# Performance work log

Measured on AMD Instinct MI355X. Metric: run time of the kernel, lower is better.

## Reference

```python
import jax, jax.numpy as jnp
import numpy as np

EPS = 1e-5
ALPHA = 0.7
N_HEADS = 20
N_KV_HEADS = 5
HEAD_DIM = 128


def bitlinear(x, w):
    # absmean ternary quantization per output row: w_t = sign(w)*(|w| > alpha*absmean)
    absw = jnp.abs(w)
    absmean = jnp.mean(absw, axis=1, keepdims=True)            # [out, 1]
    tern = jnp.sign(w) * (absw > ALPHA * absmean).astype(w.dtype)
    # (X @ pos^T - X @ neg^T) * scale == (X @ tern^T) * scale
    return jnp.einsum('...i,oi->...o', x, tern) * absmean[:, 0]


def rmsnorm(x, g):
    var = jnp.mean(jnp.square(x), axis=-1, keepdims=True)
    return x * jax.lax.rsqrt(var + EPS) * g


def rotate_half(x):
    x1, x2 = jnp.split(x, 2, axis=-1)
    return jnp.concatenate([-x2, x1], axis=-1)


def setup_inputs() -> dict:
    key = jax.random.key(0)
    ks = jax.random.split(key, 12)
    h, inter = 2560, 6912
    b, s = 1, 2048
    wscale = 1.0 / np.sqrt(h)
    return {
        'x': jax.random.normal(ks[0], (b, s, h), jnp.float32),
        'cos': jax.random.uniform(ks[1], (1, 1, s, HEAD_DIM), jnp.float32),
        'sin': jax.random.uniform(ks[2], (1, 1, s, HEAD_DIM), jnp.float32),
        'q_w': jax.random.normal(ks[3], (h, h), jnp.float32) * wscale,
        'k_w': jax.random.normal(ks[4], (N_KV_HEADS * HEAD_DIM, h), jnp.float32) * wscale,
        'v_w': jax.random.normal(ks[5], (N_KV_HEADS * HEAD_DIM, h), jnp.float32) * wscale,
        'o_w': jax.random.normal(ks[6], (h, h), jnp.float32) * wscale,
        'gate_w': jax.random.normal(ks[7], (inter, h), jnp.float32) * wscale,
        'up_w': jax.random.normal(ks[8], (inter, h), jnp.float32) * wscale,
        'down_w': jax.random.normal(ks[9], (h, inter), jnp.float32) / np.sqrt(inter),
        'ln1_w': jnp.ones((h,), jnp.float32),
        'ln2_w': jnp.ones((h,), jnp.float32),
    }


def reference(x, cos, sin, q_w, k_w, v_w, o_w, gate_w, up_w, down_w, ln1_w, ln2_w):
    b, s, hdim = x.shape
    residual = x
    h = rmsnorm(x, ln1_w)

    q = bitlinear(h, q_w).reshape(b, s, N_HEADS, HEAD_DIM).transpose(0, 2, 1, 3)
    k = bitlinear(h, k_w).reshape(b, s, N_KV_HEADS, HEAD_DIM).transpose(0, 2, 1, 3)
    v = bitlinear(h, v_w).reshape(b, s, N_KV_HEADS, HEAD_DIM).transpose(0, 2, 1, 3)

    # RoPE
    q = q * cos + rotate_half(q) * sin
    k = k * cos + rotate_half(k) * sin

    # GQA: repeat_interleave kv heads
    n_rep = N_HEADS // N_KV_HEADS
    k = jnp.repeat(k, n_rep, axis=1)
    v = jnp.repeat(v, n_rep, axis=1)

    scale = 1.0 / np.sqrt(HEAD_DIM)
    attn = jnp.einsum('bhqd,bhkd->bhqk', q, k) * scale
    attn = jax.nn.softmax(attn, axis=-1)
    o = jnp.einsum('bhqk,bhkd->bhqd', attn, v)
    o = o.transpose(0, 2, 1, 3).reshape(b, s, hdim)

    x = residual + bitlinear(o, o_w)

    residual = x
    h = rmsnorm(x, ln2_w)
    gate = jnp.square(jax.nn.relu(bitlinear(h, gate_w)))  # relu^2
    x = residual + bitlinear(gate * bitlinear(h, up_w), down_w)
    return x
```

## Files before the change

kernel.cpp:

```cpp
#include <hip/hip_runtime.h>
#include <hip/hip_bf16.h>

typedef unsigned short u16;
typedef short bf16x8 __attribute__((ext_vector_type(8)));
typedef float f32x4 __attribute__((ext_vector_type(4)));

__device__ __forceinline__ u16 f2b(float f) {
    union { __hip_bfloat16 h; u16 u; } cv;
    cv.h = __float2bfloat16(f);
    return cv.u;
}
__device__ __forceinline__ float b2f(u16 u) {
    union { u16 u; __hip_bfloat16 h; } cv;
    cv.u = u;
    return __bfloat162float(cv.h);
}

__device__ __forceinline__ void g2l16(const void* g, void* l) {
    __builtin_amdgcn_global_load_lds(
        (const __attribute__((address_space(1))) unsigned int*)g,
        (__attribute__((address_space(3))) unsigned int*)l, 16, 0, 0);
}

template <int EPT>
__global__ __launch_bounds__(256) void quant_kernel(const float* __restrict__ W,
                                                    u16* __restrict__ T,
                                                    float* __restrict__ scales, int K) {
    const int row = blockIdx.x, tid = threadIdx.x;
    const float* wr = W + (size_t)row * K;
    float v[EPT];
    float s = 0.f;
#pragma unroll
    for (int i = 0; i < EPT; ++i) { v[i] = wr[tid + i * 256]; s += fabsf(v[i]); }
#pragma unroll
    for (int d = 1; d < 64; d <<= 1) s += __shfl_xor(s, d);
    __shared__ float red[4];
    if ((tid & 63) == 0) red[tid >> 6] = s;
    __syncthreads();
    const float absmean = (red[0] + red[1] + red[2] + red[3]) / (float)K;
    const float thr = 0.7f * absmean;
    u16* tr = T + (size_t)row * K;
#pragma unroll
    for (int i = 0; i < EPT; ++i) {
        float w = v[i];
        float t = (fabsf(w) > thr) ? ((w > 0.f) ? 1.f : -1.f) : 0.f;
        tr[tid + i * 256] = f2b(t);
    }
    if (tid == 0) scales[row] = absmean;
}

__global__ __launch_bounds__(256) void rmsnorm_kernel(const float* __restrict__ x,
                                                      const float* __restrict__ g,
                                                      u16* __restrict__ o) {
    const int row = blockIdx.x, tid = threadIdx.x;
    const float* xr = x + (size_t)row * 2560;
    float v[10];
    float s = 0.f;
#pragma unroll
    for (int i = 0; i < 10; ++i) { v[i] = xr[tid + i * 256]; s += v[i] * v[i]; }
#pragma unroll
    for (int d = 1; d < 64; d <<= 1) s += __shfl_xor(s, d);
    __shared__ float red[4];
    if ((tid & 63) == 0) red[tid >> 6] = s;
    __syncthreads();
    const float total = red[0] + red[1] + red[2] + red[3];
    const float rs = rsqrtf(total * (1.f / 2560.f) + 1e-5f);
    u16* orow = o + (size_t)row * 2560;
#pragma unroll
    for (int i = 0; i < 10; ++i) orow[tid + i * 256] = f2b(v[i] * rs * g[tid + i * 256]);
}

template <int MODE>
__global__ __launch_bounds__(512, 4) void gemm_bt(const u16* __restrict__ A,
                                                  const u16* __restrict__ B,
                                                  const float* __restrict__ scale,
                                                  const float* __restrict__ res,
                                                  void* __restrict__ outp,
                                                  int M, int N, int K) {
    __shared__ __align__(16) u16 sA[128 * 64];
    __shared__ __align__(16) u16 sB[128 * 64];
    const int tid = threadIdx.x;
    const int wave = tid >> 6, lane = tid & 63;
    const int lane15 = lane & 15, quad = lane >> 4;
    const int m0 = blockIdx.x * 128, n0 = blockIdx.y * 128;
    const int wm = wave >> 2, wn = wave & 3;

    f32x4 acc[4][2] = {};

    const int r0 = wave * 8 + (lane >> 3);
    const int gcc = (lane & 7) ^ (lane >> 3);
    const size_t aoff = (size_t)(m0 + r0) * K + gcc * 8;
    const size_t boff = (size_t)(n0 + r0) * K + gcc * 8;
    char* ldsA = (char*)sA + wave * 1024;
    char* ldsB = (char*)sB + wave * 1024;
    const int sw = lane15 & 7;

    for (int kt = 0; kt < K; kt += 64) {
        g2l16(A + aoff + kt, ldsA);
        g2l16(A + aoff + (size_t)64 * K + kt, ldsA + 8192);
        g2l16(B + boff + kt, ldsB);
        g2l16(B + boff + (size_t)64 * K + kt, ldsB + 8192);
        __syncthreads();
#pragma unroll
        for (int kc = 0; kc < 2; ++kc) {
            const int pc = ((kc * 4 + quad) ^ sw) * 8;
            bf16x8 af[4], bfr[2];
#pragma unroll
            for (int f = 0; f < 4; ++f)
                af[f] = *(const bf16x8*)&sA[(wm * 64 + f * 16 + lane15) * 64 + pc];
#pragma unroll
            for (int f = 0; f < 2; ++f)
                bfr[f] = *(const bf16x8*)&sB[(wn * 32 + f * 16 + lane15) * 64 + pc];
#pragma unroll
            for (int i = 0; i < 4; ++i)
#pragma unroll
                for (int j = 0; j < 2; ++j)
                    acc[i][j] = __builtin_amdgcn_mfma_f32_16x16x32_bf16(af[i], bfr[j], acc[i][j], 0, 0, 0);
        }
        __syncthreads();
    }

#pragma unroll
    for (int j = 0; j < 2; ++j) {
        const int c = n0 + wn * 32 + j * 16 + lane15;
        const float sc = scale[c];
#pragma unroll
        for (int i = 0; i < 4; ++i) {
            const int rbase = m0 + wm * 64 + i * 16 + quad * 4;
#pragma unroll
            for (int r = 0; r < 4; ++r) {
                const float vv = acc[i][j][r] * sc;
                const size_t idx = (size_t)(rbase + r) * N + c;
                if (MODE == 0) ((u16*)outp)[idx] = f2b(vv);
                else           ((float*)outp)[idx] = res[idx] + vv;
            }
        }
    }
}

__global__ __launch_bounds__(256) void rope_kernel(u16* __restrict__ buf, int stride,
                                                   const float* __restrict__ cs,
                                                   const float* __restrict__ sn, int nh) {
    const int idx = blockIdx.x * 256 + threadIdx.x;
    const int d = idx & 63;
    const int h = (idx >> 6) % nh;
    const int s = idx / (64 * nh);
    const size_t base = (size_t)s * stride + h * 128;
    const float a = b2f(buf[base + d]), b = b2f(buf[base + d + 64]);
    const float c1 = cs[s * 128 + d], s1 = sn[s * 128 + d];
    const float c2 = cs[s * 128 + d + 64], s2 = sn[s * 128 + d + 64];
    buf[base + d] = f2b(a * c1 - b * s1);
    buf[base + d + 64] = f2b(b * c2 + a * s2);
}

__global__ __launch_bounds__(256) void transpose_v_kernel(const u16* __restrict__ V, int stride,
                                                          u16* __restrict__ VT) {
    __shared__ u16 t[128 * 66];
    const int tid = threadIdx.x;
    const int h = blockIdx.y, s0 = blockIdx.x * 64;
#pragma unroll
    for (int i = 0; i < 32; ++i) {
        const int idx = tid + i * 256;
        const int r = idx >> 7, c = idx & 127;
        t[c * 66 + r] = V[(size_t)(s0 + r) * stride + h * 128 + c];
    }
    __syncthreads();
#pragma unroll
    for (int i = 0; i < 32; ++i) {
        const int idx = tid + i * 256;
        const int d = idx >> 6, s = idx & 63;
        VT[((size_t)h * 128 + d) * 2048 + s0 + s] = t[d * 66 + s];
    }
}

__global__ __launch_bounds__(256, 3) void flash_kernel(const u16* __restrict__ Q, int qs,
                                                       const u16* __restrict__ Kb,
                                                       const u16* __restrict__ VT,
                                                       u16* __restrict__ O) {
    __shared__ __align__(16) u16 sQ[64 * 128];
    __shared__ __align__(16) u16 sK[2][32 * 128];
    __shared__ __align__(16) u16 sV[2][128 * 32];
    const int tid = threadIdx.x, wave = tid >> 6, lane = tid & 63;
    const int lane15 = lane & 15, quad = lane >> 4;
    const int head = blockIdx.y, q0 = blockIdx.x * 64, kvh = head >> 2;
    const int sw = lane15 & 7;

    const int rk = wave * 4 + (lane >> 4);
    const int gk = (lane & 15) ^ (rk & 7);
    const u16* kbase = Kb + (size_t)rk * qs + kvh * 128 + gk * 8;
    const int rv = wave * 16 + (lane >> 2);
    const int gv = (lane & 3) ^ ((lane >> 3) & 3);
    const u16* vbase = VT + ((size_t)kvh * 128 + rv) * 2048 + gv * 8;

    auto stage = [&](int k0, int b) {
        char* dK = (char*)(&sK[b][0]) + wave * 1024;
        char* dV = (char*)(&sV[b][0]) + wave * 1024;
#pragma unroll
        for (int s = 0; s < 2; ++s) {
            g2l16(kbase + ((size_t)k0 + s * 16) * qs, dK + s * 4096);
            g2l16(vbase + (size_t)s * 64 * 2048 + k0, dV + s * 4096);
        }
    };

    {
        const int rq = wave * 4 + (lane >> 4);
        const int gq = (lane & 15) ^ (rq & 7);
        const u16* src = Q + (size_t)(q0 + rq) * qs + head * 128 + gq * 8;
        char* dst = (char*)sQ + wave * 1024;
#pragma unroll
        for (int s = 0; s < 4; ++s)
            g2l16(src + (size_t)s * 16 * qs, dst + s * 4096);
        stage(0, 0);
    }
    __syncthreads();
    bf16x8 qf[4];
#pragma unroll
    for (int kc = 0; kc < 4; ++kc)
        qf[kc] = *(const bf16x8*)&sQ[(wave * 16 + lane15) * 128 + ((kc * 4 + quad) ^ sw) * 8];

    float m_i[4], lp[4];
    f32x4 o_acc[8] = {};
#pragma unroll
    for (int r = 0; r < 4; ++r) { m_i[r] = -1e30f; lp[r] = 0.f; }

    const float sl2e = 0.088388347648318447f * 1.4426950408889634f;
    const float THR = 8.0f;
    u16* sP = sQ;

    for (int t = 0; t < 64; ++t) {
        const int buf = t & 1;
        if (t < 63) stage((t + 1) * 32, buf ^ 1);
        const u16* sKb = &sK[buf][0];
        const u16* sVb = &sV[buf][0];

        f32x4 sacc[2] = {};
        __builtin_amdgcn_s_setprio(1);
#pragma unroll
        for (int nf = 0; nf < 2; ++nf)
#pragma unroll
            for (int kc = 0; kc < 4; ++kc) {
                const bf16x8 kf = *(const bf16x8*)&sKb[(nf * 16 + lane15) * 128 + ((kc * 4 + quad) ^ sw) * 8];
                sacc[nf] = __builtin_amdgcn_mfma_f32_16x16x32_bf16(qf[kc], kf, sacc[nf], 0, 0, 0);
            }
        __builtin_amdgcn_s_setprio(0);

        float mx[4];
#pragma unroll
        for (int r = 0; r < 4; ++r) {
            float v0 = sacc[0][r] * sl2e, v1 = sacc[1][r] * sl2e;
            sacc[0][r] = v0; sacc[1][r] = v1;
            float m0 = fmaxf(v0, v1);
#pragma unroll
            for (int d = 1; d < 16; d <<= 1) m0 = fmaxf(m0, __shfl_xor(m0, d));
            mx[r] = m0;
        }
        const int upd = (mx[0] > m_i[0] + THR) | (mx[1] > m_i[1] + THR) |
                        (mx[2] > m_i[2] + THR) | (mx[3] > m_i[3] + THR);
        if (__any(upd)) {
#pragma unroll
            for (int r = 0; r < 4; ++r) {
                const float mnew = fmaxf(m_i[r], mx[r]);
                const float alpha = exp2f(m_i[r] - mnew);
                m_i[r] = mnew;
                lp[r] *= alpha;
#pragma unroll
                for (int nf = 0; nf < 8; ++nf) o_acc[nf][r] *= alpha;
            }
        }
#pragma unroll
        for (int r = 0; r < 4; ++r) {
            const float m = m_i[r];
            const float p0 = exp2f(sacc[0][r] - m), p1 = exp2f(sacc[1][r] - m);
            sacc[0][r] = p0; sacc[1][r] = p1;
            lp[r] += p0 + p1;
        }

#pragma unroll
        for (int nf = 0; nf < 2; ++nf) {
            const int pcol = nf * 16 + lane15;
#pragma unroll
            for (int r = 0; r < 4; ++r)
                sP[(wave * 16 + quad * 4 + r) * 40 + pcol] = f2b(sacc[nf][r]);
        }

        const bf16x8 pf = *(const bf16x8*)&sP[(wave * 16 + lane15) * 40 + quad * 8];
        __builtin_amdgcn_s_setprio(1);
#pragma unroll
        for (int nf = 0; nf < 8; ++nf) {
            const bf16x8 vf = *(const bf16x8*)&sVb[(nf * 16 + lane15) * 32 +
                                                   ((quad ^ ((lane15 >> 1) & 3))) * 8];
            o_acc[nf] = __builtin_amdgcn_mfma_f32_16x16x32_bf16(pf, vf, o_acc[nf], 0, 0, 0);
        }
        __builtin_amdgcn_s_setprio(0);
        __syncthreads();
    }

#pragma unroll
    for (int r = 0; r < 4; ++r) {
        float lt = lp[r];
#pragma unroll
        for (int d = 1; d < 16; d <<= 1) lt += __shfl_xor(lt, d);
        const float inv = 1.f / lt;
        const int row = q0 + wave * 16 + quad * 4 + r;
        u16* orow = O + (size_t)row * 2560 + head * 128;
#pragma unroll
        for (int nf = 0; nf < 8; ++nf)
            orow[nf * 16 + lane15] = f2b(o_acc[nf][r] * inv);
    }
}

__global__ __launch_bounds__(256) void glu_kernel(u16* __restrict__ g, const u16* __restrict__ u) {
    const size_t i = ((size_t)blockIdx.x * 256 + threadIdx.x) * 8;
    bf16x8 gv = *(const bf16x8*)(g + i);
    bf16x8 uv = *(const bf16x8*)(u + i);
    bf16x8 ov;
#pragma unroll
    for (int j = 0; j < 8; ++j) {
        float x = b2f((u16)gv[j]);
        x = fmaxf(x, 0.f);
        ov[j] = (short)f2b(x * x * b2f((u16)uv[j]));
    }
    *(bf16x8*)(g + i) = ov;
}

extern "C" void kernel_launch(void* const* d_in, const int* in_sizes, int n_in,
                              void* d_out, int out_size, void* d_ws, size_t ws_size,
                              hipStream_t stream) {
    (void)in_sizes; (void)n_in; (void)out_size; (void)ws_size;
    const float* x      = (const float*)d_in[0];
    const float* cosb   = (const float*)d_in[1];
    const float* sinb   = (const float*)d_in[2];
    const float* q_w    = (const float*)d_in[3];
    const float* k_w    = (const float*)d_in[4];
    const float* v_w    = (const float*)d_in[5];
    const float* o_w    = (const float*)d_in[6];
    const float* gate_w = (const float*)d_in[7];
    const float* up_w   = (const float*)d_in[8];
    const float* down_w = (const float*)d_in[9];
    const float* ln1    = (const float*)d_in[10];
    const float* ln2    = (const float*)d_in[11];

    char* w = (char*)d_ws;
    size_t off = 0;
    auto nxt = [&](size_t sz) { char* p = w + off; off += sz; return p; };
    u16*   TQ = (u16*)nxt(13107200);
    u16*   TK = (u16*)nxt(3276800);
    u16*   TV = (u16*)nxt(3276800);
    u16*   TO = (u16*)nxt(13107200);
    u16*   TB = (u16*)nxt(35389440);
    float* SC = (float*)nxt(91136);
    u16*   H  = (u16*)nxt(10485760);
    u16*   QKV = (u16*)nxt(15728640);
    u16*   VT = (u16*)nxt(2621440);
    float* XM = (float*)nxt(20971520);
    u16*   G  = (u16*)nxt(28311552);
    u16*   U  = TQ;

    quant_kernel<10><<<2560, 256, 0, stream>>>(q_w, TQ, SC + 0, 2560);
    quant_kernel<10><<<640, 256, 0, stream>>>(k_w, TK, SC + 2560, 2560);
    quant_kernel<10><<<640, 256, 0, stream>>>(v_w, TV, SC + 3200, 2560);
    quant_kernel<10><<<2560, 256, 0, stream>>>(o_w, TO, SC + 3840, 2560);
    rmsnorm_kernel<<<2048, 256, 0, stream>>>(x, ln1, H);
    gemm_bt<0><<<dim3(16, 30), 512, 0, stream>>>(H, TQ, SC + 0, nullptr, QKV, 2048, 3840, 2560);
    rope_kernel<<<10240, 256, 0, stream>>>(QKV, 3840, cosb, sinb, 20);
    rope_kernel<<<2560, 256, 0, stream>>>(QKV + 2560, 3840, cosb, sinb, 5);
    transpose_v_kernel<<<dim3(32, 5), 256, 0, stream>>>(QKV + 3200, 3840, VT);
    flash_kernel<<<dim3(32, 20), 256, 0, stream>>>(QKV, 3840, QKV + 2560, VT, H);
    gemm_bt<1><<<dim3(16, 20), 512, 0, stream>>>(H, TO, SC + 3840, x, XM, 2048, 2560, 2560);

    rmsnorm_kernel<<<2048, 256, 0, stream>>>(XM, ln2, H);
    quant_kernel<10><<<6912, 256, 0, stream>>>(gate_w, TB, SC + 6400, 2560);
    gemm_bt<0><<<dim3(16, 54), 512, 0, stream>>>(H, TB, SC + 6400, nullptr, G, 2048, 6912, 2560);
    quant_kernel<10><<<6912, 256, 0, stream>>>(up_w, TB, SC + 13312, 2560);
    gemm_bt<0><<<dim3(16, 54), 512, 0, stream>>>(H, TB, SC + 13312, nullptr, U, 2048, 6912, 2560);
    glu_kernel<<<6912, 256, 0, stream>>>(G, U);
    quant_kernel<27><<<2560, 256, 0, stream>>>(down_w, TB, SC + 20224, 6912);
    gemm_bt<1><<<dim3(16, 20), 512, 0, stream>>>(G, TB, SC + 20224, XM, (float*)d_out, 2048, 2560, 6912);
}
```

Measured before the change: 875.7 us.

## Use 32x32 MFMA in GEMM, fuse relu² gating into up GEMM, vectorize quant/rmsnorm

Three changes. The GEMM inner loop moves from 16x16x32 to 32x32x16 bf16 MFMA with one f32x16 accumulator per 32-row tile, which cuts the number of LDS fragment loads per MFMA. A new epilogue mode fuses relu² of the gate output and the elementwise product into the up-projection GEMM, so the separate GLU kernel and the U buffer round trip go away. The quant and rmsnorm kernels switch to float4 loads and packed stores. The risk is a less coalesced epilogue store pattern with 32-lane column strides, and reading and writing G in place inside the GEMM epilogue.

Result: no change. 861.7 us (-1.6%).

```diff
diff --git a/kernel.cpp b/kernel.cpp
--- a/kernel.cpp
+++ b/kernel.cpp
@@ -4,6 +4,9 @@
 typedef unsigned short u16;
 typedef short bf16x8 __attribute__((ext_vector_type(8)));
 typedef float f32x4 __attribute__((ext_vector_type(4)));
+typedef float f32x16 __attribute__((ext_vector_type(16)));
+typedef float f4 __attribute__((ext_vector_type(4)));
+typedef unsigned short u16x4 __attribute__((ext_vector_type(4)));
 
 __device__ __forceinline__ u16 f2b(float f) {
     union { __hip_bfloat16 h; u16 u; } cv;
@@ -22,16 +25,23 @@
         (__attribute__((address_space(3))) unsigned int*)l, 16, 0, 0);
 }
 
-template <int EPT>
+template <int NV4, int NS>
 __global__ __launch_bounds__(256) void quant_kernel(const float* __restrict__ W,
                                                     u16* __restrict__ T,
                                                     float* __restrict__ scales, int K) {
     const int row = blockIdx.x, tid = threadIdx.x;
     const float* wr = W + (size_t)row * K;
-    float v[EPT];
+    f4 v[NV4];
+    float vs[NS];
     float s = 0.f;
 #pragma unroll
-    for (int i = 0; i < EPT; ++i) { v[i] = wr[tid + i * 256]; s += fabsf(v[i]); }
+    for (int j = 0; j < NV4; ++j) {
+        v[j] = ((const f4*)wr)[tid + j * 256];
+#pragma unroll
+        for (int e = 0; e < 4; ++e) s += fabsf(v[j][e]);
+    }
+#pragma unroll
+    for (int j = 0; j < NS; ++j) { vs[j] = wr[NV4 * 1024 + j * 256 + tid]; s += fabsf(vs[j]); }
 #pragma unroll
     for (int d = 1; d < 64; d <<= 1) s += __shfl_xor(s, d);
     __shared__ float red[4];
@@ -41,10 +51,19 @@
     const float thr = 0.7f * absmean;
     u16* tr = T + (size_t)row * K;
 #pragma unroll
-    for (int i = 0; i < EPT; ++i) {
-        float w = v[i];
-        float t = (fabsf(w) > thr) ? ((w > 0.f) ? 1.f : -1.f) : 0.f;
-        tr[tid + i * 256] = f2b(t);
+    for (int j = 0; j < NV4; ++j) {
+        u16x4 o;
+#pragma unroll
+        for (int e = 0; e < 4; ++e) {
+            const float w = v[j][e];
+            o[e] = (fabsf(w) > thr) ? ((w > 0.f) ? (u16)0x3F80 : (u16)0xBF80) : (u16)0;
+        }
+        ((u16x4*)tr)[tid + j * 256] = o;
+    }
+#pragma unroll
+    for (int j = 0; j < NS; ++j) {
+        const float w = vs[j];
+        tr[NV4 * 1024 + j * 256 + tid] = (fabsf(w) > thr) ? ((w > 0.f) ? (u16)0x3F80 : (u16)0xBF80) : (u16)0;
     }
     if (tid == 0) scales[row] = absmean;
 }
@@ -54,10 +73,17 @@
                                                       u16* __restrict__ o) {
     const int row = blockIdx.x, tid = threadIdx.x;
     const float* xr = x + (size_t)row * 2560;
-    float v[10];
+    f4 v[2];
+    float vs[2];
     float s = 0.f;
 #pragma unroll
-    for (int i = 0; i < 10; ++i) { v[i] = xr[tid + i * 256]; s += v[i] * v[i]; }
+    for (int j = 0; j < 2; ++j) {
+        v[j] = ((const f4*)xr)[tid + j * 256];
+#pragma unroll
+        for (int e = 0; e < 4; ++e) s += v[j][e] * v[j][e];
+    }
+#pragma unroll
+    for (int j = 0; j < 2; ++j) { vs[j] = xr[2048 + j * 256 + tid]; s += vs[j] * vs[j]; }
 #pragma unroll
     for (int d = 1; d < 64; d <<= 1) s += __shfl_xor(s, d);
     __shared__ float red[4];
@@ -67,25 +93,34 @@
     const float rs = rsqrtf(total * (1.f / 2560.f) + 1e-5f);
     u16* orow = o + (size_t)row * 2560;
 #pragma unroll
-    for (int i = 0; i < 10; ++i) orow[tid + i * 256] = f2b(v[i] * rs * g[tid + i * 256]);
+    for (int j = 0; j < 2; ++j) {
+        const f4 gv = ((const f4*)g)[tid + j * 256];
+        u16x4 ov;
+#pragma unroll
+        for (int e = 0; e < 4; ++e) ov[e] = f2b(v[j][e] * rs * gv[e]);
+        ((u16x4*)orow)[tid + j * 256] = ov;
+    }
+#pragma unroll
+    for (int j = 0; j < 2; ++j)
+        orow[2048 + j * 256 + tid] = f2b(vs[j] * rs * g[2048 + j * 256 + tid]);
 }
 
 template <int MODE>
 __global__ __launch_bounds__(512, 4) void gemm_bt(const u16* __restrict__ A,
                                                   const u16* __restrict__ B,
                                                   const float* __restrict__ scale,
-                                                  const float* __restrict__ res,
+                                                  const float* res,
                                                   void* __restrict__ outp,
                                                   int M, int N, int K) {
     __shared__ __align__(16) u16 sA[128 * 64];
     __shared__ __align__(16) u16 sB[128 * 64];
     const int tid = threadIdx.x;
     const int wave = tid >> 6, lane = tid & 63;
-    const int lane15 = lane & 15, quad = lane >> 4;
+    const int l31 = lane & 31, half = lane >> 5;
     const int m0 = blockIdx.x * 128, n0 = blockIdx.y * 128;
     const int wm = wave >> 2, wn = wave & 3;
 
-    f32x4 acc[4][2] = {};
+    f32x16 acc[2] = {};
 
     const int r0 = wave * 8 + (lane >> 3);
     const int gcc = (lane & 7) ^ (lane >> 3);
@@ -93,7 +128,10 @@
     const size_t boff = (size_t)(n0 + r0) * K + gcc * 8;
     char* ldsA = (char*)sA + wave * 1024;
     char* ldsB = (char*)sB + wave * 1024;
-    const int sw = lane15 & 7;
+    const int swz = l31 & 7;
+    const int arow0 = (wm * 64 + l31) * 64;
+    const int arow1 = (wm * 64 + 32 + l31) * 64;
+    const int brow = (wn * 32 + l31) * 64;
 
     for (int kt = 0; kt < K; kt += 64) {
         g2l16(A + aoff + kt, ldsA);
@@ -102,37 +140,32 @@
         g2l16(B + boff + (size_t)64 * K + kt, ldsB + 8192);
         __syncthreads();
 #pragma unroll
-        for (int kc = 0; kc < 2; ++kc) {
-            const int pc = ((kc * 4 + quad) ^ sw) * 8;
-            bf16x8 af[4], bfr[2];
-#pragma unroll
-            for (int f = 0; f < 4; ++f)
-                af[f] = *(const bf16x8*)&sA[(wm * 64 + f * 16 + lane15) * 64 + pc];
-#pragma unroll
-            for (int f = 0; f < 2; ++f)
-                bfr[f] = *(const bf16x8*)&sB[(wn * 32 + f * 16 + lane15) * 64 + pc];
-#pragma unroll
-            for (int i = 0; i < 4; ++i)
-#pragma unroll
-                for (int j = 0; j < 2; ++j)
-                    acc[i][j] = __builtin_amdgcn_mfma_f32_16x16x32_bf16(af[i], bfr[j], acc[i][j], 0, 0, 0);
+        for (int ks = 0; ks < 4; ++ks) {
+            const int pc = ((ks * 2 + half) ^ swz) * 8;
+            const bf16x8 bfr = *(const bf16x8*)&sB[brow + pc];
+            const bf16x8 a0 = *(const bf16x8*)&sA[arow0 + pc];
+            const bf16x8 a1 = *(const bf16x8*)&sA[arow1 + pc];
+            acc[0] = __builtin_amdgcn_mfma_f32_32x32x16_bf16(a0, bfr, acc[0], 0, 0, 0);
+            acc[1] = __builtin_amdgcn_mfma_f32_32x32x16_bf16(a1, bfr, acc[1], 0, 0, 0);
         }
         __syncthreads();
     }
 
-#pragma unroll
-    for (int j = 0; j < 2; ++j) {
-        const int c = n0 + wn * 32 + j * 16 + lane15;
-        const float sc = scale[c];
-#pragma unroll
-        for (int i = 0; i < 4; ++i) {
-            const int rbase = m0 + wm * 64 + i * 16 + quad * 4;
-#pragma unroll
-            for (int r = 0; r < 4; ++r) {
-                const float vv = acc[i][j][r] * sc;
-                const size_t idx = (size_t)(rbase + r) * N + c;
-                if (MODE == 0) ((u16*)outp)[idx] = f2b(vv);
-                else           ((float*)outp)[idx] = res[idx] + vv;
+    const int c = n0 + wn * 32 + l31;
+    const float sc = scale[c];
+#pragma unroll
+    for (int mt = 0; mt < 2; ++mt) {
+        const int rb = m0 + wm * 64 + mt * 32 + 4 * half;
+#pragma unroll
+        for (int r = 0; r < 16; ++r) {
+            const int row = rb + (r & 3) + 8 * (r >> 2);
+            const float vv = acc[mt][r] * sc;
+            const size_t idx = (size_t)row * N + c;
+            if (MODE == 0)      ((u16*)outp)[idx] = f2b(vv);
+            else if (MODE == 1) ((float*)outp)[idx] = res[idx] + vv;
+            else {
+                const float gg = fmaxf(b2f(((const u16*)res)[idx]), 0.f);
+                ((u16*)outp)[idx] = f2b(gg * gg * vv);
             }
         }
     }
@@ -307,20 +340,6 @@
         for (int nf = 0; nf < 8; ++nf)
             orow[nf * 16 + lane15] = f2b(o_acc[nf][r] * inv);
     }
-}
-
-__global__ __launch_bounds__(256) void glu_kernel(u16* __restrict__ g, const u16* __restrict__ u) {
-    const size_t i = ((size_t)blockIdx.x * 256 + threadIdx.x) * 8;
-    bf16x8 gv = *(const bf16x8*)(g + i);
-    bf16x8 uv = *(const bf16x8*)(u + i);
-    bf16x8 ov;
-#pragma unroll
-    for (int j = 0; j < 8; ++j) {
-        float x = b2f((u16)gv[j]);
-        x = fmaxf(x, 0.f);
-        ov[j] = (short)f2b(x * x * b2f((u16)uv[j]));
-    }
-    *(bf16x8*)(g + i) = ov;
 }
 
 extern "C" void kernel_launch(void* const* d_in, const int* in_sizes, int n_in,
@@ -354,12 +373,11 @@
     u16*   VT = (u16*)nxt(2621440);
     float* XM = (float*)nxt(20971520);
     u16*   G  = (u16*)nxt(28311552);
-    u16*   U  = TQ;
-
-    quant_kernel<10><<<2560, 256, 0, stream>>>(q_w, TQ, SC + 0, 2560);
-    quant_kernel<10><<<640, 256, 0, stream>>>(k_w, TK, SC + 2560, 2560);
-    quant_kernel<10><<<640, 256, 0, stream>>>(v_w, TV, SC + 3200, 2560);
-    quant_kernel<10><<<2560, 256, 0, stream>>>(o_w, TO, SC + 3840, 2560);
+
+    quant_kernel<2, 2><<<2560, 256, 0, stream>>>(q_w, TQ, SC + 0, 2560);
+    quant_kernel<2, 2><<<640, 256, 0, stream>>>(k_w, TK, SC + 2560, 2560);
+    quant_kernel<2, 2><<<640, 256, 0, stream>>>(v_w, TV, SC + 3200, 2560);
+    quant_kernel<2, 2><<<2560, 256, 0, stream>>>(o_w, TO, SC + 3840, 2560);
     rmsnorm_kernel<<<2048, 256, 0, stream>>>(x, ln1, H);
     gemm_bt<0><<<dim3(16, 30), 512, 0, stream>>>(H, TQ, SC + 0, nullptr, QKV, 2048, 3840, 2560);
     rope_kernel<<<10240, 256, 0, stream>>>(QKV, 3840, cosb, sinb, 20);
@@ -369,11 +387,10 @@
     gemm_bt<1><<<dim3(16, 20), 512, 0, stream>>>(H, TO, SC + 3840, x, XM, 2048, 2560, 2560);
 
     rmsnorm_kernel<<<2048, 256, 0, stream>>>(XM, ln2, H);
-    quant_kernel<10><<<6912, 256, 0, stream>>>(gate_w, TB, SC + 6400, 2560);
+    quant_kernel<2, 2><<<6912, 256, 0, stream>>>(gate_w, TB, SC + 6400, 2560);
     gemm_bt<0><<<dim3(16, 54), 512, 0, stream>>>(H, TB, SC + 6400, nullptr, G, 2048, 6912, 2560);
-    quant_kernel<10><<<6912, 256, 0, stream>>>(up_w, TB, SC + 13312, 2560);
-    gemm_bt<0><<<dim3(16, 54), 512, 0, stream>>>(H, TB, SC + 13312, nullptr, U, 2048, 6912, 2560);
-    glu_kernel<<<6912, 256, 0, stream>>>(G, U);
-    quant_kernel<27><<<2560, 256, 0, stream>>>(down_w, TB, SC + 20224, 6912);
+    quant_kernel<2, 2><<<6912, 256, 0, stream>>>(up_w, TB, SC + 13312, 2560);
+    gemm_bt<2><<<dim3(16, 54), 512, 0, stream>>>(H, TB, SC + 13312, (const float*)G, G, 2048, 6912, 2560);
+    quant_kernel<6, 3><<<2560, 256, 0, stream>>>(down_w, TB, SC + 20224, 6912);
     gemm_bt<1><<<dim3(16, 20), 512, 0, stream>>>(G, TB, SC + 20224, XM, (float*)d_out, 2048, 2560, 6912);
 }
```
